# Kernel optimization log

Measured on AMD Instinct MI355X. Metric: run time of the kernel, lower is better.

Reference implementation:

```python
import jax, jax.numpy as jnp
import numpy as np
from jax import lax

B, T, E, D = 16, 4096, 512, 128
LOCAL_SIZE, SUMMARY_FREQ = 64, 32
LN_EPS = 1e-5


def setup_inputs() -> dict:
    key = jax.random.key(0)
    ks = jax.random.split(key, 12)
    p = lambda k, s: 0.1 * jax.random.normal(k, s, jnp.float32) + 0.01
    return {
        "x": jax.random.normal(ks[0], (B, T, E), jnp.float32),
        "local_state_control": p(ks[1], (D, D)),
        "local_input_influence": p(ks[2], (E, D)),
        "local_blend_shaper": p(ks[3], (D, D)),
        "global_summary_state_control": p(ks[4], (D, D)),
        "global_summary_state_influence": p(ks[5], (E, D)),
        "global_summary_output_shaper": p(ks[6], (D, D)),
        "global_state_control": p(ks[7], (D, D)),
        "global_input_influence": p(ks[8], (E, D)),
        "global_output_shaper": p(ks[9], (D, E)),
        "ln_gamma": jnp.ones((D,), jnp.float32),
        "ln_beta": jnp.zeros((D,), jnp.float32),
        "lin_w": 0.02 * jax.random.normal(ks[10], (E, E), jnp.float32),
        "lin_b": jnp.zeros((E,), jnp.float32),
        "local_size": LOCAL_SIZE,
        "summary_frequency": SUMMARY_FREQ,
    }


def _ln(h, g, b):
    m = jnp.mean(h, -1, keepdims=True)
    v = jnp.var(h, -1, keepdims=True)
    return (h - m) * lax.rsqrt(v + LN_EPS) * g + b


def reference(x, local_state_control, local_input_influence, local_blend_shaper,
              global_summary_state_control, global_summary_state_influence,
              global_summary_output_shaper, global_state_control,
              global_input_influence, global_output_shaper,
              ln_gamma, ln_beta, lin_w, lin_b, local_size, summary_frequency):
    # Dropout layers are identity in inference mode.
    Bb, Tt, Ee = x.shape
    Dd = ln_gamma.shape[0]
    t_idx = jnp.arange(Tt)

    # ---- Local windowed recurrence, vectorized across all timesteps t. ----
    # Original: for each t, local_state starts at 0 and consumes tokens
    # t-1, t-2, ..., max(0, t-local_size) in that (reverse) order.
    # We scan over window offset j; at step j, timestep t consumes token t-1-j.
    x_pad = jnp.pad(x, ((0, 0), (local_size, 0), (0, 0)))  # pad front of time axis

    def local_step(S, j):  # S: [B, T, D]
        # X[:, t, :] == x[:, t-1-j, :] (zeros where out of range)
        X = lax.dynamic_slice_in_dim(x_pad, local_size - 1 - j, Tt, axis=1)
        valid = (t_idx >= j + 1)[None, :, None]  # token index t-1-j >= 0
        S_new = _ln(S @ local_state_control + X @ local_input_influence, ln_gamma, ln_beta)
        return jnp.where(valid, S_new, S), None

    S0 = jnp.zeros((Bb, Tt, Dd), x.dtype)
    S_local, _ = lax.scan(local_step, S0, jnp.arange(local_size))
    blended = S_local @ local_blend_shaper  # [B, T, D]

    # ---- Global sequential recurrence over time. ----
    is_summary = (t_idx % summary_frequency) == (summary_frequency - 1)

    def gstep(carry, inp):
        g, summ = carry  # [B, D], [B, D]
        x_t, loc_t, flag = inp
        g = _ln(g @ global_state_control + x_t @ global_input_influence + loc_t + summ,
                ln_gamma, ln_beta)
        out_t = g @ global_output_shaper  # [B, E]
        summ_new = _ln(summ @ global_summary_state_control +
                       out_t @ global_summary_state_influence,
                       ln_gamma, ln_beta) @ global_summary_output_shaper
        summ = jnp.where(flag, summ_new, summ)
        return (g, summ), out_t

    init = (jnp.zeros((Bb, Dd), x.dtype), jnp.zeros((Bb, Dd), x.dtype))
    _, outs = lax.scan(gstep, init,
                       (x.transpose(1, 0, 2), blended.transpose(1, 0, 2), is_summary))
    out = outs.transpose(1, 0, 2)  # [B, T, E]
    return out @ lin_w.T + lin_b
```

## Files before the change

kernel.cpp:

```cpp
#include <hip/hip_runtime.h>
#include <stdint.h>


typedef unsigned short u16;
typedef unsigned int   u32;
typedef __attribute__((ext_vector_type(8))) short bf16x8;
typedef __attribute__((ext_vector_type(4))) float f32x4;
typedef __attribute__((ext_vector_type(2))) u32   u32x2;
typedef __attribute__((ext_vector_type(4))) u32   u32x4;

#define MFMA16(a,b,c) __builtin_amdgcn_mfma_f32_16x16x32_bf16((a),(b),(c),0,0,0)

static constexpr int T_SEQ   = 4096;
static constexpr int CHUNK_C = 64;
static constexpr int WARM_C  = 256;

__device__ __forceinline__ u32 bf16rne(float x){
  u32 u = __float_as_uint(x);
  return (u + 0x7FFFu + ((u >> 16) & 1u)) >> 16;
}
__device__ __forceinline__ u32 rne_hi(u32 u){
  return u + 0x7FFFu + ((u >> 16) & 1u);
}
__device__ __forceinline__ u32 pk2(float lo, float hi){
  return __builtin_amdgcn_perm(rne_hi(__float_as_uint(hi)),
                               rne_hi(__float_as_uint(lo)), 0x07060302u);
}
__device__ __forceinline__ u32 cvtpk(float lo, float hi){
  u32 r;
  asm("v_cvt_pk_bf16_f32 %0, %1, %2" : "=v"(r) : "v"(lo), "v"(hi));
  return r;
}
__device__ __forceinline__ float bflo(u32 p){ return __uint_as_float(p << 16); }
__device__ __forceinline__ float bfhi(u32 p){ return __uint_as_float(p & 0xFFFF0000u); }

__device__ __forceinline__ bf16x8 mk8(u32x2 a, u32x2 b){
  union { u32 u[4]; bf16x8 v; } t;
  t.u[0] = a.x; t.u[1] = a.y; t.u[2] = b.x; t.u[3] = b.y;
  return t.v;
}

__device__ __forceinline__ void gload_lds16(const float* g, void* l){
  __builtin_amdgcn_global_load_lds(
      (const __attribute__((address_space(1))) void*)g,
      (__attribute__((address_space(3))) void*)l, 16, 0, 0);
}

__device__ __forceinline__ int kperm(int s){
  return (s & 0xE0) | ((s & 4) << 2) | ((s >> 1) & 0x0C) | (s & 3);
}

__device__ __forceinline__ float xsum4(float v){
#if __has_builtin(__builtin_amdgcn_permlane16_swap) && __has_builtin(__builtin_amdgcn_permlane32_swap)
  typedef __attribute__((ext_vector_type(2))) unsigned pl2u;
  pl2u a = __builtin_amdgcn_permlane16_swap(__float_as_uint(v), __float_as_uint(v),
                                            false, false);
  float s = __uint_as_float(a.x) + __uint_as_float(a.y);
  pl2u b = __builtin_amdgcn_permlane32_swap(__float_as_uint(s), __float_as_uint(s),
                                            false, false);
  return __uint_as_float(b.x) + __uint_as_float(b.y);
#else
  v += __shfl_xor(v, 16, 64);
  v += __shfl_xor(v, 32, 64);
  return v;
#endif
}

__device__ __forceinline__ void ln_stats(const f32x4 (&C)[8], float &rs, float &mr){
  float s4[8], q4[8];
#pragma unroll
  for (int mt = 0; mt < 8; ++mt){
    float a = C[mt][0] + C[mt][1], b = C[mt][2] + C[mt][3];
    s4[mt] = a + b;
    float p = C[mt][0]*C[mt][0]; p = __builtin_fmaf(C[mt][1], C[mt][1], p);
    float r = C[mt][2]*C[mt][2]; r = __builtin_fmaf(C[mt][3], C[mt][3], r);
    q4[mt] = p + r;
  }
  float s  = ((s4[0]+s4[1])+(s4[2]+s4[3])) + ((s4[4]+s4[5])+(s4[6]+s4[7]));
  float ss = ((q4[0]+q4[1])+(q4[2]+q4[3])) + ((q4[4]+q4[5])+(q4[6]+q4[7]));
  s  = xsum4(s);
  ss = xsum4(ss);
  float mean = s * 0.0078125f;
  float var  = __builtin_fmaf(ss, 0.0078125f, -mean*mean);
  rs = rsqrtf(var + 1e-5f);
  mr = mean * rs;
}

__global__ void prep_fold(const float* lsc, const float* lbs, const float* gsc,
                          const float* gssc, const float* gsos,
                          const float* lii, const float* gii, const float* gamma,
                          u16* WlscA, u16* WlbsA, u16* WgcA,
                          u16* WsscA, u16* WssoA, u16* WcatA){
  int id = blockIdx.x * 256 + threadIdx.x;
  if (id < 81920){
    int m = id >> 14;
    int r = id & 16383;
    int j = r >> 7, k = r & 127;
    int kd = kperm(k);
    float g = gamma[kd];
    float v = 0.f; u16* dst = WlscA;
    switch (m){
      case 0: v = g * lsc[kd*128 + j];  dst = WlscA; break;
      case 1: v = g * lbs[kd*128 + j];  dst = WlbsA; break;
      case 2: v = g * gsc[kd*128 + j];  dst = WgcA;  break;
      case 3: v =     gssc[kd*128 + j]; dst = WsscA; break;
      default: v = g * gsos[kd*128 + j]; dst = WssoA; break;
    }
    dst[j*128 + k] = (u16)bf16rne(v);
  } else {
    int r = id - 81920;
    int m = r >> 9, k = r & 511;
    float v = (m < 128) ? lii[k*128 + m] : gii[k*128 + (m - 128)];
    WcatA[m*512 + k] = (u16)bf16rne(v);
  }
}

__global__ void prep_dot(const float* gos, const float* gssi, const float* linw,
                         const float* gamma, const float* beta,
                         u16* Wsi2A, u16* WfinA, float* bout){
  int id = blockIdx.x * 256 + threadIdx.x;
  if (id < 16384){
    int j = id >> 7, k = id & 127;
    int kd = kperm(k);
    float s = 0.f;
    for (int e = 0; e < 512; ++e) s += gos[kd*512 + e] * gssi[e*128 + j];
    Wsi2A[j*128 + k] = (u16)bf16rne(gamma[kd] * s);
  } else if (id < 81920){
    int r = id - 16384;
    int f = r >> 7, k = r & 127;
    float s = 0.f;
    for (int e = 0; e < 512; ++e) s += gos[k*512 + e] * linw[f*512 + e];
    WfinA[f*128 + k] = (u16)bf16rne(gamma[k] * s);
  } else {
    int e = id - 81920;
    float s = 0.f;
    for (int d = 0; d < 128; ++d) s += beta[d] * gos[d*512 + e];
    bout[e] = s;
  }
}

__global__ void prep_vec(const float* lsc, const float* lbs, const float* gsc,
                         const float* gsos, const float* gssi,
                         const float* linw, const float* linb,
                         const float* gamma, const float* beta, const float* bout,
                         float* biaslsc, float* badd, float* bsi, float* bso,
                         float* bfin, u16* y0){
  int t = threadIdx.x;
  if (t < 128){
    float s1 = 0.f, s2 = 0.f, s3 = 0.f;
    for (int k = 0; k < 128; ++k){
      float bk = beta[k];
      s1 += bk * lsc[k*128 + t];
      s2 += bk * (lbs[k*128 + t] + gsc[k*128 + t]);
      s3 += bk * gsos[k*128 + t];
    }
    biaslsc[t] = s1; badd[t] = s2; bso[t] = s3;
    float s4 = 0.f;
    for (int e = 0; e < 512; ++e) s4 += bout[e] * gssi[e*128 + t];
    bsi[t] = s4;
    y0[t] = (u16)bf16rne(-beta[t] / gamma[t]);
  }
  float s5 = 0.f;
  for (int e = 0; e < 512; ++e) s5 += bout[e] * linw[t*512 + e];
  bfin[t] = s5 + linb[t];
}

__global__ __launch_bounds__(256, 2)
void stageA(const float* x, const u16* WcatA, const float* biaslsc,
            u16* U, float* R){
  __shared__ u16 Wl[256 * 40];
  __shared__ u16 Xl[64 * 40];
  const int t0 = blockIdx.x * 64;
  const int tid = threadIdx.x;
  const int w = tid >> 6, lane = tid & 63, ln = lane & 15, q = lane >> 4;

  f32x4 C[4][4];
#pragma unroll
  for (int a = 0; a < 4; ++a)
#pragma unroll
    for (int b = 0; b < 4; ++b) C[a][b] = (f32x4)0.f;

  const int ti = tid >> 2, p = tid & 3;
  for (int kc = 0; kc < 16; ++kc){
    {
      const u16* src = WcatA + tid*512 + kc*32;
#pragma unroll
      for (int i = 0; i < 4; ++i)
        *(u32x4*)&Wl[tid*40 + i*8] = *(const u32x4*)(src + i*8);
      const float* xs = x + (size_t)(t0 + ti)*512 + kc*32 + p*8;
      f32x4 xa = *(const f32x4*)(xs);
      f32x4 xb = *(const f32x4*)(xs + 4);
      u32x4 xw = { pk2(xa[0],xa[1]), pk2(xa[2],xa[3]),
                   pk2(xb[0],xb[1]), pk2(xb[2],xb[3]) };
      *(u32x4*)&Xl[ti*40 + p*8] = xw;
    }
    __syncthreads();
    bf16x8 Af[4], Bf[4];
#pragma unroll
    for (int mt = 0; mt < 4; ++mt)
      Af[mt] = *(const bf16x8*)&Wl[(16*(4*w + mt) + ln)*40 + 8*q];
#pragma unroll
    for (int nt = 0; nt < 4; ++nt)
      Bf[nt] = *(const bf16x8*)&Xl[(16*nt + ln)*40 + 8*q];
#pragma unroll
    for (int mt = 0; mt < 4; ++mt)
#pragma unroll
      for (int nt = 0; nt < 4; ++nt)
        C[mt][nt] = MFMA16(Af[mt], Bf[nt], C[mt][nt]);
    __syncthreads();
  }
#pragma unroll
  for (int mt = 0; mt < 4; ++mt){
    int mg = 64*w + 16*mt + 4*q;
    if (mg < 128){
      f32x4 bl = *(const f32x4*)(biaslsc + mg);
#pragma unroll
      for (int nt = 0; nt < 4; ++nt){
        int row = t0 + 16*nt + ln;
        u32x2 pv = { pk2(C[mt][nt][0] + bl[0], C[mt][nt][1] + bl[1]),
                     pk2(C[mt][nt][2] + bl[2], C[mt][nt][3] + bl[3]) };
        *(u32x2*)(U + (size_t)row*128 + mg) = pv;
      }
    } else {
      int d = mg - 128;
#pragma unroll
      for (int nt = 0; nt < 4; ++nt){
        int row = t0 + 16*nt + ln;
        *(f32x4*)(R + (size_t)row*128 + d) = C[mt][nt];
      }
    }
  }
}

__global__ __launch_bounds__(256, 2)
void stageB(const u16* U, const u16* WlscA, const u16* WlbsA,
            const float* badd, const u16* y0, float* R){
  __shared__ u16 Ul[128 * 136];
  const int b = blockIdx.x >> 6, ch = blockIdx.x & 63;
  const int t0 = ch * 64;
  const int tid = threadIdx.x;
  const int w = tid >> 6, lane = tid & 63, ln = lane & 15, q = lane >> 4;
  const int rowb = b * T_SEQ;

  for (int u = tid; u < 2048; u += 256){
    int r = u >> 4, c = u & 15;
    int rg = t0 - 64 + r; if (rg < 0) rg = 0;
    u32x4 v = *(const u32x4*)(U + (size_t)(rowb + rg)*128 + c*8);
    *(u32x4*)&Ul[r*136 + c*8] = v;
  }
  u32x2 yp[8];
#pragma unroll
  for (int mt = 0; mt < 8; ++mt)
    yp[mt] = *(const u32x2*)(y0 + 16*mt + 4*q);
  __syncthreads();

  bf16x8 A[8][4];
#pragma unroll
  for (int mt = 0; mt < 8; ++mt)
#pragma unroll
    for (int kt = 0; kt < 4; ++kt)
      A[mt][kt] = *(const bf16x8*)(WlscA + (16*mt + ln)*128 + 32*kt + 8*q);

  const int tl = t0 + 16*w + ln;
  for (int j = 0; j < 64; ++j){
    const int lr = 64 + 16*w + ln - 1 - j;
    f32x4 C[8];
#pragma unroll
    for (int mt = 0; mt < 8; ++mt){
      u32x2 uv = *(const u32x2*)&Ul[lr*136 + 16*mt + 4*q];
      C[mt][0] = bflo(uv.x); C[mt][1] = bfhi(uv.x);
      C[mt][2] = bflo(uv.y); C[mt][3] = bfhi(uv.y);
    }
    bf16x8 Bf[4];
#pragma unroll
    for (int kt = 0; kt < 4; ++kt)
      Bf[kt] = mk8(yp[2*kt], yp[2*kt+1]);
#pragma unroll
    for (int mt = 0; mt < 8; ++mt)
#pragma unroll
      for (int kt = 0; kt < 4; ++kt)
        C[mt] = MFMA16(A[mt][kt], Bf[kt], C[mt]);
    float rs, mr; ln_stats(C, rs, mr);
    if (tl >= j + 1){
#pragma unroll
      for (int mt = 0; mt < 8; ++mt){
        yp[mt].x = pk2(__builtin_fmaf(C[mt][0], rs, -mr),
                       __builtin_fmaf(C[mt][1], rs, -mr));
        yp[mt].y = pk2(__builtin_fmaf(C[mt][2], rs, -mr),
                       __builtin_fmaf(C[mt][3], rs, -mr));
      }
    }
  }

#pragma unroll
  for (int mt = 0; mt < 8; ++mt)
#pragma unroll
    for (int kt = 0; kt < 4; ++kt)
      A[mt][kt] = *(const bf16x8*)(WlbsA + (16*mt + ln)*128 + 32*kt + 8*q);
  bf16x8 Bf[4];
#pragma unroll
  for (int kt = 0; kt < 4; ++kt)
    Bf[kt] = mk8(yp[2*kt], yp[2*kt+1]);
  f32x4 C[8];
#pragma unroll
  for (int mt = 0; mt < 8; ++mt)
    C[mt] = *(const f32x4*)(badd + 16*mt + 4*q);
#pragma unroll
  for (int mt = 0; mt < 8; ++mt)
#pragma unroll
    for (int kt = 0; kt < 4; ++kt)
      C[mt] = MFMA16(A[mt][kt], Bf[kt], C[mt]);
#pragma unroll
  for (int mt = 0; mt < 8; ++mt){
    float* rp = R + (size_t)(rowb + tl)*128 + 16*mt + 4*q;
    f32x4 rv = *(const f32x4*)rp;
    *(f32x4*)rp = C[mt] + rv;
  }
}

__global__ __launch_bounds__(64, 1)
void stageC(const float* R, const u16* WgcA, const u16* WsscA,
            const u16* Wsi2A, const u16* WssoA,
            const float* bsi, const float* bso, const u16* y0, u16* Y,
            u16* dump){
  __shared__ f32x4 ring[2048];
  const int c0 = blockIdx.x * CHUNK_C;
  const int ts = (c0 - WARM_C > 0) ? (c0 - WARM_C) : 0;
  const int te = c0 + CHUNK_C;
  const int lane = threadIdx.x, ln = lane & 15, q = lane >> 4;
  const int rb = ln * T_SEQ;
  const u32 lbase = (u32)lane * 16u;

  bf16x8 A[8][4];
#pragma unroll
  for (int mt = 0; mt < 8; ++mt)
#pragma unroll
    for (int kt = 0; kt < 4; ++kt)
      A[mt][kt] = *(const bf16x8*)(WgcA + (16*mt + ln)*128 + 32*kt + 8*q);

  u32x2 ypb[4][8];
#pragma unroll
  for (int mt = 0; mt < 8; ++mt){
    u32x2 v = *(const u32x2*)(y0 + 16*mt + 4*q);
    ypb[0][mt] = v; ypb[1][mt] = v; ypb[2][mt] = v; ypb[3][mt] = v;
  }

#pragma unroll
  for (int mt = 0; mt < 8; ++mt){
    asm volatile("" :: "v"(A[mt][0]), "v"(A[mt][1]), "v"(A[mt][2]), "v"(A[mt][3]));
    asm volatile("" :: "v"(ypb[0][mt]), "v"(ypb[1][mt]),
                       "v"(ypb[2][mt]), "v"(ypb[3][mt]));
  }

  f32x4 summ[8];
#pragma unroll
  for (int mt = 0; mt < 8; ++mt) summ[mt] = (f32x4)0.f;

  u16* const dumpl = dump + (size_t)blockIdx.x * 8192 + (size_t)lane * 128;

#pragma unroll
  for (int p = 0; p < 4; ++p){
    const float* ra = R + (size_t)(rb + ts + p)*128 + 4*q;
#pragma unroll
    for (int mt = 0; mt < 8; ++mt)
      gload_lds16(ra + 16*mt, (char*)ring + p*8192 + mt*1024);
  }
  asm volatile("s_waitcnt vmcnt(0)" ::: "memory");
  __builtin_amdgcn_sched_barrier(0);

  const int ngroups = (te - ts) >> 2;
  for (int g = 0; g < ngroups; ++g){
    const int tb = ts + g*4;
#pragma unroll
    for (int p = 0; p < 4; ++p){
      const int tt = tb + p;

      asm volatile("s_waitcnt vmcnt(48)"
        :: "v"(ypb[p][0]), "v"(ypb[p][1]), "v"(ypb[p][2]), "v"(ypb[p][3]),
           "v"(ypb[p][4]), "v"(ypb[p][5]), "v"(ypb[p][6]), "v"(ypb[p][7])
        : "memory");
      __builtin_amdgcn_sched_barrier(0);

      u32x4 D[8];
#pragma unroll
      for (int mt = 0; mt < 8; ++mt)
        asm volatile("ds_read_b128 %0, %1 offset:%c2"
                     : "=v"(D[mt]) : "v"(lbase), "i"(p*8192 + mt*1024));
      asm volatile("s_waitcnt lgkmcnt(0)" ::: "memory");
      __builtin_amdgcn_sched_barrier(0);

      {
        int tn = tt + 4; if (tn > te - 1) tn = te - 1;
        const float* ra = R + (size_t)(rb + tn)*128 + 4*q;
#pragma unroll
        for (int mt = 0; mt < 8; ++mt)
          gload_lds16(ra + 16*mt, (char*)ring + p*8192 + mt*1024);
      }

      f32x4 C[8];
#pragma unroll
      for (int mt = 0; mt < 8; ++mt){
        union { u32x4 u; f32x4 f; } cv; cv.u = D[mt];
        C[mt] = cv.f + summ[mt];
      }

      bf16x8 Bf[4];
#pragma unroll
      for (int kt = 0; kt < 4; ++kt)
        Bf[kt] = mk8(ypb[(p+3)&3][2*kt], ypb[(p+3)&3][2*kt+1]);
#pragma unroll
      for (int mt = 0; mt < 8; ++mt)
#pragma unroll
        for (int kt = 0; kt < 4; ++kt)
          C[mt] = MFMA16(A[mt][kt], Bf[kt], C[mt]);
      float rs, mr; ln_stats(C, rs, mr);
#pragma unroll
      for (int mt = 0; mt < 8; ++mt){
        ypb[p][mt].x = cvtpk(__builtin_fmaf(C[mt][0], rs, -mr),
                             __builtin_fmaf(C[mt][1], rs, -mr));
        ypb[p][mt].y = cvtpk(__builtin_fmaf(C[mt][2], rs, -mr),
                             __builtin_fmaf(C[mt][3], rs, -mr));
      }

      u16* yt = (tt >= c0)
        ? (u16*)((char*)Y + (((size_t)(rb + tt)) << 8) + 8*q)
        : dumpl;
#pragma unroll
      for (int mt = 0; mt < 8; ++mt)
        asm volatile("global_store_dwordx2 %0, %1, off offset:%c2"
                     :: "v"(yt), "v"(ypb[p][mt]), "i"(mt*32) : "memory");

      if (p == 3 && ((tt & 31) == 31)){
        bf16x8 Sf[4], Yf[4];
        u32x2 sp[8];
#pragma unroll
        for (int mt = 0; mt < 8; ++mt){
          sp[mt].x = cvtpk(summ[mt][0], summ[mt][1]);
          sp[mt].y = cvtpk(summ[mt][2], summ[mt][3]);
        }
#pragma unroll
        for (int kt = 0; kt < 4; ++kt){
          Sf[kt] = mk8(sp[2*kt], sp[2*kt+1]);
          Yf[kt] = mk8(ypb[3][2*kt], ypb[3][2*kt+1]);
        }
        f32x4 Cz[8];
#pragma unroll
        for (int mt = 0; mt < 8; ++mt)
          Cz[mt] = *(const f32x4*)(bsi + 16*mt + 4*q);
#pragma unroll
        for (int mt = 0; mt < 8; ++mt)
#pragma unroll
          for (int kt = 0; kt < 4; ++kt){
            bf16x8 Aw = *(const bf16x8*)(WsscA + (16*mt + ln)*128 + 32*kt + 8*q);
            Cz[mt] = MFMA16(Aw, Sf[kt], Cz[mt]);
          }
#pragma unroll
        for (int mt = 0; mt < 8; ++mt)
#pragma unroll
          for (int kt = 0; kt < 4; ++kt){
            bf16x8 Aw = *(const bf16x8*)(Wsi2A + (16*mt + ln)*128 + 32*kt + 8*q);
            Cz[mt] = MFMA16(Aw, Yf[kt], Cz[mt]);
          }
        float rz, mz; ln_stats(Cz, rz, mz);
        u32x2 zp[8];
#pragma unroll
        for (int mt = 0; mt < 8; ++mt){
          zp[mt].x = cvtpk(__builtin_fmaf(Cz[mt][0], rz, -mz),
                           __builtin_fmaf(Cz[mt][1], rz, -mz));
          zp[mt].y = cvtpk(__builtin_fmaf(Cz[mt][2], rz, -mz),
                           __builtin_fmaf(Cz[mt][3], rz, -mz));
        }
        bf16x8 Zf[4];
#pragma unroll
        for (int kt = 0; kt < 4; ++kt)
          Zf[kt] = mk8(zp[2*kt], zp[2*kt+1]);
        f32x4 Cs[8];
#pragma unroll
        for (int mt = 0; mt < 8; ++mt)
          Cs[mt] = *(const f32x4*)(bso + 16*mt + 4*q);
#pragma unroll
        for (int mt = 0; mt < 8; ++mt)
#pragma unroll
          for (int kt = 0; kt < 4; ++kt){
            bf16x8 Aw = *(const bf16x8*)(WssoA + (16*mt + ln)*128 + 32*kt + 8*q);
            Cs[mt] = MFMA16(Aw, Zf[kt], Cs[mt]);
          }
#pragma unroll
        for (int mt = 0; mt < 8; ++mt) summ[mt] = Cs[mt];
      }
    }
  }
  asm volatile("s_waitcnt vmcnt(0)" ::: "memory");
}

__global__ __launch_bounds__(256, 2)
void stageD(const u16* Y, const u16* WfinA, const float* bfin, float* Out){
  __shared__ u16 Yl[32 * 136];
  const size_t row0 = (size_t)blockIdx.x * 32;
  const int tid = threadIdx.x;
  const int w = tid >> 6, lane = tid & 63, ln = lane & 15, q = lane >> 4;

  for (int u = tid; u < 512; u += 256){
    int r = u >> 4, c = u & 15;
    u32x4 v = *(const u32x4*)(Y + (row0 + r)*128 + c*8);
    *(u32x4*)&Yl[r*136 + c*8] = v;
  }
  __syncthreads();

  bf16x8 A[8][4];
#pragma unroll
  for (int mt = 0; mt < 8; ++mt)
#pragma unroll
    for (int kt = 0; kt < 4; ++kt)
      A[mt][kt] = *(const bf16x8*)(WfinA + (size_t)(128*w + 16*mt + ln)*128 + 32*kt + 8*q);
  bf16x8 Bf[2][4];
#pragma unroll
  for (int nt = 0; nt < 2; ++nt)
#pragma unroll
    for (int kt = 0; kt < 4; ++kt)
      Bf[nt][kt] = *(const bf16x8*)&Yl[(16*nt + ln)*136 + 32*kt + 8*q];
  f32x4 C[8][2];
#pragma unroll
  for (int mt = 0; mt < 8; ++mt)
#pragma unroll
    for (int nt = 0; nt < 2; ++nt) C[mt][nt] = (f32x4)0.f;
#pragma unroll
  for (int mt = 0; mt < 8; ++mt)
#pragma unroll
    for (int nt = 0; nt < 2; ++nt)
#pragma unroll
      for (int kt = 0; kt < 4; ++kt)
        C[mt][nt] = MFMA16(A[mt][kt], Bf[nt][kt], C[mt][nt]);
#pragma unroll
  for (int mt = 0; mt < 8; ++mt){
    f32x4 bv = *(const f32x4*)(bfin + 128*w + 16*mt + 4*q);
#pragma unroll
    for (int nt = 0; nt < 2; ++nt){
      f32x4 o = C[mt][nt] + bv;
      *(f32x4*)(Out + (row0 + 16*nt + ln)*512 + 128*w + 16*mt + 4*q) = o;
    }
  }
}

extern "C" void kernel_launch(void* const* d_in, const int* in_sizes, int n_in,
                              void* d_out, int out_size, void* d_ws, size_t ws_size,
                              hipStream_t stream) {
  const float* x    = (const float*)d_in[0];
  const float* lsc  = (const float*)d_in[1];
  const float* lii  = (const float*)d_in[2];
  const float* lbs  = (const float*)d_in[3];
  const float* gssc = (const float*)d_in[4];
  const float* gssi = (const float*)d_in[5];
  const float* gsos = (const float*)d_in[6];
  const float* gsc  = (const float*)d_in[7];
  const float* gii  = (const float*)d_in[8];
  const float* gos  = (const float*)d_in[9];
  const float* gam  = (const float*)d_in[10];
  const float* bet  = (const float*)d_in[11];
  const float* linw = (const float*)d_in[12];
  const float* linb = (const float*)d_in[13];
  (void)in_sizes; (void)n_in; (void)out_size; (void)ws_size;

  char* w8 = (char*)d_ws;
  float* R       = (float*)(w8);
  u16*   U       = (u16*)  (w8 + 33554432);
  u16*   Y       = (u16*)  (w8 + 50331648);
  u16*   WcatA   = (u16*)  (w8 + 67108864);
  u16*   WlscA   = (u16*)  (w8 + 67371008);
  u16*   WlbsA   = (u16*)  (w8 + 67403776);
  u16*   WgcA    = (u16*)  (w8 + 67436544);
  u16*   WsscA   = (u16*)  (w8 + 67469312);
  u16*   WssoA   = (u16*)  (w8 + 67502080);
  u16*   Wsi2A   = (u16*)  (w8 + 67534848);
  u16*   WfinA   = (u16*)  (w8 + 67567616);
  float* biaslsc = (float*)(w8 + 67698688);
  float* badd    = (float*)(w8 + 67699200);
  float* bsi     = (float*)(w8 + 67699712);
  float* bso     = (float*)(w8 + 67700224);
  float* bout    = (float*)(w8 + 67700736);
  float* bfin    = (float*)(w8 + 67702784);
  u16*   y0      = (u16*)  (w8 + 67704832);

  prep_fold<<<832, 256, 0, stream>>>(lsc, lbs, gsc, gssc, gsos, lii, gii, gam,
                                     WlscA, WlbsA, WgcA, WsscA, WssoA, WcatA);
  prep_dot <<<322, 256, 0, stream>>>(gos, gssi, linw, gam, bet, Wsi2A, WfinA, bout);
  prep_vec <<<1, 512, 0, stream>>>(lsc, lbs, gsc, gsos, gssi, linw, linb,
                                   gam, bet, bout, biaslsc, badd, bsi, bso, bfin, y0);
  stageA<<<1024, 256, 0, stream>>>(x, WcatA, biaslsc, U, R);
  stageB<<<1024, 256, 0, stream>>>(U, WlscA, WlbsA, badd, y0, R);
  stageC<<<64, 64, 0, stream>>>(R, WgcA, WsscA, Wsi2A, WssoA, bsi, bso, y0, Y, U);
  stageD<<<2048, 256, 0, stream>>>(Y, WfinA, bfin, (float*)d_out);
}
```

Baseline: 983.0 us.

## Interleave R time-major across batch and skip dummy stores in warmup steps

The R buffer written by stageA and stageB is re-laid out as [t][b][d], so stageC's per-timestep prefetch of 16 batch rows reads one contiguous 8 KB block. The LDS ring gets padded strides so reads stay conflict-free under the new layout. The warmup loop is split from the output loop so warmup steps no longer issue dummy global stores, with vmcnt thresholds adjusted to match. This adds more strided writes in stageA/B and fragile hand-tuned waitcnt counts.

```diff
diff --git a/kernel.cpp b/kernel.cpp
--- a/kernel.cpp
+++ b/kernel.cpp
@@ -84,6 +84,68 @@
   float var  = __builtin_fmaf(ss, 0.0078125f, -mean*mean);
   rs = rsqrtf(var + 1e-5f);
   mr = mean * rs;
+}
+
+__device__ __forceinline__ void summary_update(
+    f32x4 (&summ)[8], const u32x2 (&yb)[8],
+    const u16* WsscA, const u16* Wsi2A, const u16* WssoA,
+    const float* bsi, const float* bso, int ln, int q){
+  bf16x8 Sf[4], Yf[4];
+  u32x2 sp[8];
+#pragma unroll
+  for (int mt = 0; mt < 8; ++mt){
+    sp[mt].x = cvtpk(summ[mt][0], summ[mt][1]);
+    sp[mt].y = cvtpk(summ[mt][2], summ[mt][3]);
+  }
+#pragma unroll
+  for (int kt = 0; kt < 4; ++kt){
+    Sf[kt] = mk8(sp[2*kt], sp[2*kt+1]);
+    Yf[kt] = mk8(yb[2*kt], yb[2*kt+1]);
+  }
+  f32x4 Cz[8];
+#pragma unroll
+  for (int mt = 0; mt < 8; ++mt)
+    Cz[mt] = *(const f32x4*)(bsi + 16*mt + 4*q);
+#pragma unroll
+  for (int mt = 0; mt < 8; ++mt)
+#pragma unroll
+    for (int kt = 0; kt < 4; ++kt){
+      bf16x8 Aw = *(const bf16x8*)(WsscA + (16*mt + ln)*128 + 32*kt + 8*q);
+      Cz[mt] = MFMA16(Aw, Sf[kt], Cz[mt]);
+    }
+#pragma unroll
+  for (int mt = 0; mt < 8; ++mt)
+#pragma unroll
+    for (int kt = 0; kt < 4; ++kt){
+      bf16x8 Aw = *(const bf16x8*)(Wsi2A + (16*mt + ln)*128 + 32*kt + 8*q);
+      Cz[mt] = MFMA16(Aw, Yf[kt], Cz[mt]);
+    }
+  float rz, mz; ln_stats(Cz, rz, mz);
+  u32x2 zp[8];
+#pragma unroll
+  for (int mt = 0; mt < 8; ++mt){
+    zp[mt].x = cvtpk(__builtin_fmaf(Cz[mt][0], rz, -mz),
+                     __builtin_fmaf(Cz[mt][1], rz, -mz));
+    zp[mt].y = cvtpk(__builtin_fmaf(Cz[mt][2], rz, -mz),
+                     __builtin_fmaf(Cz[mt][3], rz, -mz));
+  }
+  bf16x8 Zf[4];
+#pragma unroll
+  for (int kt = 0; kt < 4; ++kt)
+    Zf[kt] = mk8(zp[2*kt], zp[2*kt+1]);
+  f32x4 Cs[8];
+#pragma unroll
+  for (int mt = 0; mt < 8; ++mt)
+    Cs[mt] = *(const f32x4*)(bso + 16*mt + 4*q);
+#pragma unroll
+  for (int mt = 0; mt < 8; ++mt)
+#pragma unroll
+    for (int kt = 0; kt < 4; ++kt){
+      bf16x8 Aw = *(const bf16x8*)(WssoA + (16*mt + ln)*128 + 32*kt + 8*q);
+      Cs[mt] = MFMA16(Aw, Zf[kt], Cs[mt]);
+    }
+#pragma unroll
+  for (int mt = 0; mt < 8; ++mt) summ[mt] = Cs[mt];
 }
 
 __global__ void prep_fold(const float* lsc, const float* lbs, const float* gsc,
@@ -209,6 +271,7 @@
         C[mt][nt] = MFMA16(Af[mt], Bf[nt], C[mt][nt]);
     __syncthreads();
   }
+  const int bidx = t0 >> 12;
 #pragma unroll
   for (int mt = 0; mt < 4; ++mt){
     int mg = 64*w + 16*mt + 4*q;
@@ -225,8 +288,8 @@
       int d = mg - 128;
 #pragma unroll
       for (int nt = 0; nt < 4; ++nt){
-        int row = t0 + 16*nt + ln;
-        *(f32x4*)(R + (size_t)row*128 + d) = C[mt][nt];
+        int trow = (t0 & 4095) + 16*nt + ln;
+        *(f32x4*)(R + ((size_t)(trow*16 + bidx))*128 + d) = C[mt][nt];
       }
     }
   }
@@ -312,24 +375,75 @@
       C[mt] = MFMA16(A[mt][kt], Bf[kt], C[mt]);
 #pragma unroll
   for (int mt = 0; mt < 8; ++mt){
-    float* rp = R + (size_t)(rowb + tl)*128 + 16*mt + 4*q;
+    float* rp = R + ((size_t)(tl*16 + b))*128 + 16*mt + 4*q;
     f32x4 rv = *(const f32x4*)rp;
     *(f32x4*)rp = C[mt] + rv;
   }
 }
+
+#define CSTEP(P_, TT_, WAITN_, STORE_) do {                                    \
+  asm volatile("s_waitcnt vmcnt(" #WAITN_ ")"                                  \
+    :: "v"(ypb[P_][0]), "v"(ypb[P_][1]), "v"(ypb[P_][2]), "v"(ypb[P_][3]),     \
+       "v"(ypb[P_][4]), "v"(ypb[P_][5]), "v"(ypb[P_][6]), "v"(ypb[P_][7])      \
+    : "memory");                                                               \
+  __builtin_amdgcn_sched_barrier(0);                                           \
+  u32x4 D[8];                                                                  \
+  _Pragma("unroll")                                                            \
+  for (int mt = 0; mt < 8; ++mt)                                               \
+    asm volatile("ds_read_b128 %0, %1 offset:%c2"                              \
+                 : "=v"(D[mt]) : "v"(vaddr), "i"((P_)*8320 + mt*64));          \
+  asm volatile("s_waitcnt lgkmcnt(0)" ::: "memory");                           \
+  __builtin_amdgcn_sched_barrier(0);                                           \
+  { int tn = (TT_) + 4; if (tn > te - 1) tn = te - 1;                          \
+    const float* gb = R + (size_t)tn*2048 + lane*4;                            \
+    _Pragma("unroll")                                                          \
+    for (int j = 0; j < 8; ++j)                                                \
+      gload_lds16(gb + j*256, ring + (P_)*8320 + j*1040); }                    \
+  f32x4 C[8];                                                                  \
+  _Pragma("unroll")                                                            \
+  for (int mt = 0; mt < 8; ++mt){                                              \
+    union { u32x4 u; f32x4 f; } cv; cv.u = D[mt];                              \
+    C[mt] = cv.f + summ[mt];                                                   \
+  }                                                                            \
+  bf16x8 Bf[4];                                                                \
+  _Pragma("unroll")                                                            \
+  for (int kt = 0; kt < 4; ++kt)                                               \
+    Bf[kt] = mk8(ypb[((P_)+3)&3][2*kt], ypb[((P_)+3)&3][2*kt+1]);              \
+  _Pragma("unroll")                                                            \
+  for (int mt = 0; mt < 8; ++mt)                                               \
+    _Pragma("unroll")                                                          \
+    for (int kt = 0; kt < 4; ++kt)                                             \
+      C[mt] = MFMA16(A[mt][kt], Bf[kt], C[mt]);                                \
+  float rs, mr; ln_stats(C, rs, mr);                                           \
+  _Pragma("unroll")                                                            \
+  for (int mt = 0; mt < 8; ++mt){                                              \
+    ypb[P_][mt].x = cvtpk(__builtin_fmaf(C[mt][0], rs, -mr),                   \
+                          __builtin_fmaf(C[mt][1], rs, -mr));                  \
+    ypb[P_][mt].y = cvtpk(__builtin_fmaf(C[mt][2], rs, -mr),                   \
+                          __builtin_fmaf(C[mt][3], rs, -mr));                  \
+  }                                                                            \
+  if (STORE_){                                                                 \
+    u16* yt = (u16*)((char*)Y + (((size_t)(rb + (TT_))) << 8) + 8*q);          \
+    _Pragma("unroll")                                                          \
+    for (int mt = 0; mt < 8; ++mt)                                             \
+      asm volatile("global_store_dwordx2 %0, %1, off offset:%c2"               \
+                   :: "v"(yt), "v"(ypb[P_][mt]), "i"(mt*32) : "memory");       \
+  }                                                                            \
+  if ((P_) == 3 && (((TT_) & 31) == 31))                                       \
+    summary_update(summ, ypb[3], WsscA, Wsi2A, WssoA, bsi, bso, ln, q);        \
+} while(0)
 
 __global__ __launch_bounds__(64, 1)
 void stageC(const float* R, const u16* WgcA, const u16* WsscA,
             const u16* Wsi2A, const u16* WssoA,
-            const float* bsi, const float* bso, const u16* y0, u16* Y,
-            u16* dump){
-  __shared__ f32x4 ring[2048];
+            const float* bsi, const float* bso, const u16* y0, u16* Y){
+  __shared__ __align__(16) char ring[4 * 8320];
   const int c0 = blockIdx.x * CHUNK_C;
   const int ts = (c0 - WARM_C > 0) ? (c0 - WARM_C) : 0;
   const int te = c0 + CHUNK_C;
   const int lane = threadIdx.x, ln = lane & 15, q = lane >> 4;
   const int rb = ln * T_SEQ;
-  const u32 lbase = (u32)lane * 16u;
+  const u32 vaddr = (u32)((ln >> 1)*1040 + (ln & 1)*512 + q*16);
 
   bf16x8 A[8][4];
 #pragma unroll
@@ -356,139 +470,37 @@
 #pragma unroll
   for (int mt = 0; mt < 8; ++mt) summ[mt] = (f32x4)0.f;
 
-  u16* const dumpl = dump + (size_t)blockIdx.x * 8192 + (size_t)lane * 128;
-
 #pragma unroll
   for (int p = 0; p < 4; ++p){
-    const float* ra = R + (size_t)(rb + ts + p)*128 + 4*q;
-#pragma unroll
-    for (int mt = 0; mt < 8; ++mt)
-      gload_lds16(ra + 16*mt, (char*)ring + p*8192 + mt*1024);
+    const float* gb = R + (size_t)(ts + p)*2048 + lane*4;
+#pragma unroll
+    for (int j = 0; j < 8; ++j)
+      gload_lds16(gb + j*256, ring + p*8320 + j*1040);
   }
   asm volatile("s_waitcnt vmcnt(0)" ::: "memory");
   __builtin_amdgcn_sched_barrier(0);
 
-  const int ngroups = (te - ts) >> 2;
-  for (int g = 0; g < ngroups; ++g){
+  const int nw = (c0 - ts) >> 2;
+  for (int g = 0; g < nw; ++g){
     const int tb = ts + g*4;
-#pragma unroll
-    for (int p = 0; p < 4; ++p){
-      const int tt = tb + p;
-
-      asm volatile("s_waitcnt vmcnt(48)"
-        :: "v"(ypb[p][0]), "v"(ypb[p][1]), "v"(ypb[p][2]), "v"(ypb[p][3]),
-           "v"(ypb[p][4]), "v"(ypb[p][5]), "v"(ypb[p][6]), "v"(ypb[p][7])
-        : "memory");
-      __builtin_amdgcn_sched_barrier(0);
-
-      u32x4 D[8];
-#pragma unroll
-      for (int mt = 0; mt < 8; ++mt)
-        asm volatile("ds_read_b128 %0, %1 offset:%c2"
-                     : "=v"(D[mt]) : "v"(lbase), "i"(p*8192 + mt*1024));
-      asm volatile("s_waitcnt lgkmcnt(0)" ::: "memory");
-      __builtin_amdgcn_sched_barrier(0);
-
-      {
-        int tn = tt + 4; if (tn > te - 1) tn = te - 1;
-        const float* ra = R + (size_t)(rb + tn)*128 + 4*q;
-#pragma unroll
-        for (int mt = 0; mt < 8; ++mt)
-          gload_lds16(ra + 16*mt, (char*)ring + p*8192 + mt*1024);
-      }
-
-      f32x4 C[8];
-#pragma unroll
-      for (int mt = 0; mt < 8; ++mt){
-        union { u32x4 u; f32x4 f; } cv; cv.u = D[mt];
-        C[mt] = cv.f + summ[mt];
-      }
-
-      bf16x8 Bf[4];
-#pragma unroll
-      for (int kt = 0; kt < 4; ++kt)
-        Bf[kt] = mk8(ypb[(p+3)&3][2*kt], ypb[(p+3)&3][2*kt+1]);
-#pragma unroll
-      for (int mt = 0; mt < 8; ++mt)
-#pragma unroll
-        for (int kt = 0; kt < 4; ++kt)
-          C[mt] = MFMA16(A[mt][kt], Bf[kt], C[mt]);
-      float rs, mr; ln_stats(C, rs, mr);
-#pragma unroll
-      for (int mt = 0; mt < 8; ++mt){
-        ypb[p][mt].x = cvtpk(__builtin_fmaf(C[mt][0], rs, -mr),
-                             __builtin_fmaf(C[mt][1], rs, -mr));
-        ypb[p][mt].y = cvtpk(__builtin_fmaf(C[mt][2], rs, -mr),
-                             __builtin_fmaf(C[mt][3], rs, -mr));
-      }
-
-      u16* yt = (tt >= c0)
-        ? (u16*)((char*)Y + (((size_t)(rb + tt)) << 8) + 8*q)
-        : dumpl;
-#pragma unroll
-      for (int mt = 0; mt < 8; ++mt)
-        asm volatile("global_store_dwordx2 %0, %1, off offset:%c2"
-                     :: "v"(yt), "v"(ypb[p][mt]), "i"(mt*32) : "memory");
-
-      if (p == 3 && ((tt & 31) == 31)){
-        bf16x8 Sf[4], Yf[4];
-        u32x2 sp[8];
-#pragma unroll
-        for (int mt = 0; mt < 8; ++mt){
-          sp[mt].x = cvtpk(summ[mt][0], summ[mt][1]);
-          sp[mt].y = cvtpk(summ[mt][2], summ[mt][3]);
-        }
-#pragma unroll
-        for (int kt = 0; kt < 4; ++kt){
-          Sf[kt] = mk8(sp[2*kt], sp[2*kt+1]);
-          Yf[kt] = mk8(ypb[3][2*kt], ypb[3][2*kt+1]);
-        }
-        f32x4 Cz[8];
-#pragma unroll
-        for (int mt = 0; mt < 8; ++mt)
-          Cz[mt] = *(const f32x4*)(bsi + 16*mt + 4*q);
-#pragma unroll
-        for (int mt = 0; mt < 8; ++mt)
-#pragma unroll
-          for (int kt = 0; kt < 4; ++kt){
-            bf16x8 Aw = *(const bf16x8*)(WsscA + (16*mt + ln)*128 + 32*kt + 8*q);
-            Cz[mt] = MFMA16(Aw, Sf[kt], Cz[mt]);
-          }
-#pragma unroll
-        for (int mt = 0; mt < 8; ++mt)
-#pragma unroll
-          for (int kt = 0; kt < 4; ++kt){
-            bf16x8 Aw = *(const bf16x8*)(Wsi2A + (16*mt + ln)*128 + 32*kt + 8*q);
-            Cz[mt] = MFMA16(Aw, Yf[kt], Cz[mt]);
-          }
-        float rz, mz; ln_stats(Cz, rz, mz);
-        u32x2 zp[8];
-#pragma unroll
-        for (int mt = 0; mt < 8; ++mt){
-          zp[mt].x = cvtpk(__builtin_fmaf(Cz[mt][0], rz, -mz),
-                           __builtin_fmaf(Cz[mt][1], rz, -mz));
-          zp[mt].y = cvtpk(__builtin_fmaf(Cz[mt][2], rz, -mz),
-                           __builtin_fmaf(Cz[mt][3], rz, -mz));
-        }
-        bf16x8 Zf[4];
-#pragma unroll
-        for (int kt = 0; kt < 4; ++kt)
-          Zf[kt] = mk8(zp[2*kt], zp[2*kt+1]);
-        f32x4 Cs[8];
-#pragma unroll
-        for (int mt = 0; mt < 8; ++mt)
-          Cs[mt] = *(const f32x4*)(bso + 16*mt + 4*q);
-#pragma unroll
-        for (int mt = 0; mt < 8; ++mt)
-#pragma unroll
-          for (int kt = 0; kt < 4; ++kt){
-            bf16x8 Aw = *(const bf16x8*)(WssoA + (16*mt + ln)*128 + 32*kt + 8*q);
-            Cs[mt] = MFMA16(Aw, Zf[kt], Cs[mt]);
-          }
-#pragma unroll
-        for (int mt = 0; mt < 8; ++mt) summ[mt] = Cs[mt];
-      }
-    }
+    CSTEP(0, tb+0, 24, 0);
+    CSTEP(1, tb+1, 24, 0);
+    CSTEP(2, tb+2, 24, 0);
+    CSTEP(3, tb+3, 24, 0);
+  }
+
+  {
+    CSTEP(0, c0+0, 24, 1);
+    CSTEP(1, c0+1, 24, 1);
+    CSTEP(2, c0+2, 24, 1);
+    CSTEP(3, c0+3, 24, 1);
+  }
+  for (int g = 1; g < (CHUNK_C >> 2); ++g){
+    const int tb = c0 + g*4;
+    CSTEP(0, tb+0, 48, 1);
+    CSTEP(1, tb+1, 48, 1);
+    CSTEP(2, tb+2, 48, 1);
+    CSTEP(3, tb+3, 48, 1);
   }
   asm volatile("s_waitcnt vmcnt(0)" ::: "memory");
 }
@@ -588,6 +600,6 @@
                                    gam, bet, bout, biaslsc, badd, bsi, bso, bfin, y0);
   stageA<<<1024, 256, 0, stream>>>(x, WcatA, biaslsc, U, R);
   stageB<<<1024, 256, 0, stream>>>(U, WlscA, WlbsA, badd, y0, R);
-  stageC<<<64, 64, 0, stream>>>(R, WgcA, WsscA, Wsi2A, WssoA, bsi, bso, y0, Y, U);
+  stageC<<<64, 64, 0, stream>>>(R, WgcA, WsscA, Wsi2A, WssoA, bsi, bso, y0, Y);
   stageD<<<2048, 256, 0, stream>>>(Y, WfinA, bfin, (float*)d_out);
 }
```

Result: faster. 938.8 us (-4.5%).
